# Optimization experiments

Measured on AMD Instinct MI355X. Metric: run time of the kernel, lower is better.

Reference implementation:

```python
import jax, jax.numpy as jnp
import numpy as np

N_R = 100_000   # real nodes
N_E = 1_200_000 # r2r edges
G = 4096        # graphs (= interaction nodes, one per graph)
H = 64          # hidden_dim
ND = 64         # node_dim
ED = 16         # edge_dim
L = 4           # conv_layers
TGT = 1         # target_dim
SLOPE = 0.1     # LeakyReLU negative slope used by ISATconv


def _seg_softmax(logits, seg, n):
    m = jax.ops.segment_max(logits, seg, num_segments=n)
    ex = jnp.exp(logits - m[seg])
    s = jax.ops.segment_sum(ex, seg, num_segments=n)
    return ex / s[seg]


def setup_inputs() -> dict:
    key = jax.random.key(0)
    ks = jax.random.split(key, 20)
    inp = {}
    inp['r_node'] = jax.random.normal(ks[0], (N_R, ND), jnp.float32)
    inp['i_node'] = jax.random.normal(ks[1], (G, 1), jnp.float32)
    inp['r_edge'] = jax.random.normal(ks[2], (N_E, ED), jnp.float32)
    inp['d_edge'] = jax.random.uniform(ks[3], (N_R, 1), jnp.float32)
    inp['r2r_src'] = jax.random.randint(ks[4], (N_E,), 0, N_R, jnp.int32)
    inp['r2r_dst'] = jax.random.randint(ks[5], (N_E,), 0, N_R, jnp.int32)
    inp['graph_id'] = jnp.sort(jax.random.randint(ks[6], (N_R,), 0, G, jnp.int32))
    sc = 1.0 / np.sqrt(H)
    inp['W_r'] = jax.random.normal(ks[7], (ND, H), jnp.float32) * (1.0 / np.sqrt(ND))
    inp['W_i'] = jax.random.normal(ks[8], (1, H), jnp.float32)
    inp['W_e'] = jax.random.normal(ks[9], (ED, H), jnp.float32) * (1.0 / np.sqrt(ED))
    inp['Wm'] = jax.random.normal(ks[10], (L, H, H), jnp.float32) * sc
    inp['a_s'] = jax.random.normal(ks[11], (L, H), jnp.float32) * sc
    inp['a_d'] = jax.random.normal(ks[12], (L, H), jnp.float32) * sc
    inp['a_e'] = jax.random.normal(ks[13], (L, H), jnp.float32) * sc
    inp['w_d'] = jax.random.normal(ks[14], (1,), jnp.float32)
    inp['b_d'] = jnp.zeros((1,), jnp.float32)
    inp['W_mlp'] = jax.random.normal(ks[15], (3, H, H), jnp.float32) * sc
    inp['b_mlp'] = jnp.zeros((3, H), jnp.float32)
    inp['W_out'] = jax.random.normal(ks[16], (H, TGT), jnp.float32) * sc
    inp['b_out'] = jnp.zeros((TGT,), jnp.float32)
    return inp


def reference(r_node, i_node, r_edge, d_edge, r2r_src, r2r_dst, graph_id,
              W_r, W_i, W_e, Wm, a_s, a_d, a_e, w_d, b_d,
              W_mlp, b_mlp, W_out, b_out):
    lrelu = lambda x: jax.nn.leaky_relu(x, SLOPE)
    n = r_node.shape[0]
    g = i_node.shape[0]
    # embeddings (bias-free linears)
    h = r_node @ W_r          # [N,H]
    hi = i_node @ W_i         # [G,H]
    e = r_edge @ W_e          # [E,H]
    score = None
    # ISAT attention conv layers (gather-compute-scatter), residual
    for l in range(L):
        logits = lrelu(h[r2r_src] @ a_s[l] + h[r2r_dst] @ a_d[l] + e @ a_e[l])  # [E]
        attn = _seg_softmax(logits, r2r_dst, n)
        msg = attn[:, None] * (h[r2r_src] + e)
        agg = jax.ops.segment_sum(msg, r2r_dst, num_segments=n) @ Wm[l]
        h = lrelu(h + agg)
        score = attn
    # interaction-node (d2d) mixing: gate by d_edge, gather to i-nodes, broadcast back
    gate = jax.nn.sigmoid(d_edge * w_d + b_d)                 # [N,1]
    hi = hi + jax.ops.segment_sum(gate * h, graph_id, num_segments=g)
    h = h + gate * hi[graph_id]
    # sum pooling over real-node subgraph per graph
    pooled = jax.ops.segment_sum(h, graph_id, num_segments=g)  # [G,H]
    # MLP readout: 3 hidden ReLU layers + linear output
    x = pooled
    for i in range(3):
        x = jax.nn.relu(x @ W_mlp[i] + b_mlp[i])
    return x @ W_out + b_out
```

## Files before the change

### kernel.cpp

```cpp
#include <hip/hip_runtime.h>
#include <math.h>

#define N_RN 100000
#define N_ED 1200000
#define N_G  4096
#define SCAN_CH 256
#define SCAN_NB ((N_RN + SCAN_CH - 1) / SCAN_CH)

__device__ __forceinline__ float lrelu(float x) { return x > 0.f ? x : 0.1f * x; }

__global__ void k_embed_h(const float* __restrict__ r_node,
                          const float* __restrict__ W_r,
                          const float* __restrict__ a_s0,
                          const float* __restrict__ a_d0,
                          float* __restrict__ h,
                          float* __restrict__ hs, float* __restrict__ hd) {
    __shared__ float Wl[64 * 64];
    __shared__ float arow[4][64];
    int tid = threadIdx.x;
    for (int i = tid; i < 4096; i += 256) Wl[i] = W_r[i];
    __syncthreads();
    int lane = tid & 63, w = tid >> 6;
    float asj = a_s0[lane], adj = a_d0[lane];
    int wid = blockIdx.x * 4 + w;
    int nw = gridDim.x * 4;
    for (int n = wid; n < N_RN; n += nw) {
        arow[w][lane] = r_node[(size_t)n * 64 + lane];
        float acc = 0.f;
#pragma unroll
        for (int d4 = 0; d4 < 16; ++d4) {
            float4 a = *(const float4*)&arow[w][d4 * 4];
            int d = d4 * 4;
            acc += a.x * Wl[(d + 0) * 64 + lane];
            acc += a.y * Wl[(d + 1) * 64 + lane];
            acc += a.z * Wl[(d + 2) * 64 + lane];
            acc += a.w * Wl[(d + 3) * 64 + lane];
        }
        h[(size_t)n * 64 + lane] = acc;
        float x = acc * asj, y = acc * adj;
#pragma unroll
        for (int off = 32; off; off >>= 1) {
            x += __shfl_xor(x, off, 64);
            y += __shfl_xor(y, off, 64);
        }
        if (lane == 0) { hs[n] = x; hd[n] = y; }
    }
}

__global__ void k_wewm(const float* __restrict__ W_e,
                       const float* __restrict__ Wm,
                       const float* __restrict__ a_e,
                       float* __restrict__ WeWm,
                       float* __restrict__ was_all) {
    int idx = blockIdx.x * blockDim.x + threadIdx.x;
    if (idx < 4096) {
        int l = idx >> 10, rem = idx & 1023;
        int t = rem >> 6, j = rem & 63;
        float acc = 0.f;
        for (int d = 0; d < 64; ++d)
            acc += W_e[t * 64 + d] * Wm[l * 4096 + d * 64 + j];
        WeWm[idx] = acc;
    } else {
        int r = idx - 4096;
        if (r < 64) {
            int l = r >> 4, t = r & 15;
            float acc = 0.f;
            for (int j = 0; j < 64; ++j)
                acc += W_e[t * 64 + j] * a_e[l * 64 + j];
            was_all[r] = acc;
        }
    }
}

__global__ void k_hist(const int* __restrict__ dst, int* __restrict__ deg) {
    int k = blockIdx.x * blockDim.x + threadIdx.x;
    if (k < N_ED) atomicAdd(deg + dst[k], 1);
}

__global__ void k_scan_a(const int* __restrict__ deg, int* __restrict__ bsum) {
    __shared__ int lds[SCAN_CH];
    int b = blockIdx.x, t = threadIdx.x;
    int i = b * SCAN_CH + t;
    int v = (i < N_RN) ? deg[i] : 0;
    lds[t] = v;
    __syncthreads();
    for (int d = 128; d; d >>= 1) {
        if (t < d) lds[t] += lds[t + d];
        __syncthreads();
    }
    if (t == 0) bsum[b] = lds[0];
}

__global__ void k_scan_b(int* __restrict__ bsum) {
    __shared__ int lds[512];
    int t = threadIdx.x;
    int v = (t < SCAN_NB) ? bsum[t] : 0;
    lds[t] = v;
    __syncthreads();
    for (int d = 1; d < 512; d <<= 1) {
        int u = (t >= d) ? lds[t - d] : 0;
        __syncthreads();
        lds[t] += u;
        __syncthreads();
    }
    if (t < SCAN_NB) bsum[t] = lds[t] - v;
}

__global__ void k_scan_c(const int* __restrict__ deg, const int* __restrict__ bsum,
                         int* __restrict__ off, int* __restrict__ cur) {
    __shared__ int lds[SCAN_CH];
    int b = blockIdx.x, t = threadIdx.x;
    int i = b * SCAN_CH + t;
    int v = (i < N_RN) ? deg[i] : 0;
    lds[t] = v;
    __syncthreads();
    for (int d = 1; d < SCAN_CH; d <<= 1) {
        int u = (t >= d) ? lds[t - d] : 0;
        __syncthreads();
        lds[t] += u;
        __syncthreads();
    }
    if (i < N_RN) {
        int incl = bsum[b] + lds[t];
        off[i + 1] = incl;
        cur[i] = incl - v;
        if (i == 0) off[0] = 0;
    }
}

__global__ void k_scatter(const float* __restrict__ r_edge,
                          const int* __restrict__ src, const int* __restrict__ dst,
                          int* __restrict__ cur,
                          int* __restrict__ src_perm,
                          float* __restrict__ r16_perm) {
    int k = blockIdx.x * blockDim.x + threadIdx.x;
    if (k >= N_ED) return;
    const float4* row = (const float4*)(r_edge + (size_t)k * 16);
    float4 r0 = row[0], r1 = row[1], r2 = row[2], r3 = row[3];
    int pos = atomicAdd(cur + dst[k], 1);
    src_perm[pos] = src[k];
    float4* o = (float4*)(r16_perm + (size_t)pos * 16);
    o[0] = r0; o[1] = r1; o[2] = r2; o[3] = r3;
}

__global__ void k_layer(const float* __restrict__ h_in,
                        const float* __restrict__ hs, const float* __restrict__ hd,
                        const int* __restrict__ off,
                        const int* __restrict__ src_perm,
                        const float* __restrict__ r16_perm,
                        const float* __restrict__ was_l,
                        const float* __restrict__ Wm_l,
                        const float* __restrict__ WeWm_l,
                        const float* __restrict__ a_s_n, const float* __restrict__ a_d_n,
                        float* __restrict__ h_out,
                        float* __restrict__ hs_out, float* __restrict__ hd_out) {
    __shared__ float Wl[64 * 64];
    __shared__ float Ww[16 * 64];
    __shared__ float arow[4][64];
    __shared__ float rrow[4][16];
    __shared__ float wbuf[4][64];
    __shared__ int   skbuf[4][64];
    int tid = threadIdx.x;
    for (int i = tid; i < 4096; i += 256) Wl[i] = Wm_l[i];
    for (int i = tid; i < 1024; i += 256) Ww[i] = WeWm_l[i];
    __syncthreads();
    int lane = tid & 63, w = tid >> 6;
    int g = lane >> 4, lg = lane & 15;
    float asj = a_s_n[lane], adj = a_d_n[lane];
    float wr[16];
#pragma unroll
    for (int t = 0; t < 16; ++t) wr[t] = was_l[t];
    int wid = blockIdx.x * 4 + w;
    int nw = gridDim.x * 4;
    for (int n = wid; n < N_RN; n += nw) {
        int base = off[n], end = off[n + 1];
        float hdn = hd[n];
        float m = -1e38f;
        float s = 0.f, racc = 0.f;
        float acc0 = 0.f, acc1 = 0.f, acc2 = 0.f, acc3 = 0.f;
        for (int cb = base; cb < end; cb += 64) {
            int cend = cb + 64 < end ? cb + 64 : end;
            int cnt = cend - cb;
            int pos = cb + lane;
            float lgt = -1e38f;
            int sk = 0;
            if (pos < cend) {
                sk = src_perm[pos];
                const float4* rp = (const float4*)(r16_perm + (size_t)pos * 16);
                float4 r0 = rp[0], r1 = rp[1], r2 = rp[2], r3 = rp[3];
                float ep = r0.x * wr[0] + r0.y * wr[1] + r0.z * wr[2] + r0.w * wr[3]
                         + r1.x * wr[4] + r1.y * wr[5] + r1.z * wr[6] + r1.w * wr[7]
                         + r2.x * wr[8] + r2.y * wr[9] + r2.z * wr[10] + r2.w * wr[11]
                         + r3.x * wr[12] + r3.y * wr[13] + r3.z * wr[14] + r3.w * wr[15];
                lgt = lrelu(hs[sk] + hdn + ep);
            }
            float cm = lgt;
#pragma unroll
            for (int o = 32; o; o >>= 1) cm = fmaxf(cm, __shfl_xor(cm, o, 64));
            float newm = fmaxf(m, cm);
            float scale = (m > -1e37f) ? __expf(m - newm) : 0.f;
            s *= scale; racc *= scale;
            acc0 *= scale; acc1 *= scale; acc2 *= scale; acc3 *= scale;
            m = newm;
            float wv = (pos < cend) ? __expf(lgt - m) : 0.f;
            s += wv;
            wbuf[w][lane] = wv;
            skbuf[w][lane] = sk;
            for (int c = 0; c < cnt; c += 4) {
                int e = c + g;
                if (e < cnt) {
                    float wgt = wbuf[w][e];
                    int sk2 = skbuf[w][e];
                    const float4 hv = *(const float4*)(h_in + (size_t)sk2 * 64 + (lg << 2));
                    acc0 += wgt * hv.x; acc1 += wgt * hv.y;
                    acc2 += wgt * hv.z; acc3 += wgt * hv.w;
                    racc += wgt * r16_perm[(size_t)(cb + e) * 16 + lg];
                }
            }
        }
        acc0 += __shfl_xor(acc0, 16, 64); acc0 += __shfl_xor(acc0, 32, 64);
        acc1 += __shfl_xor(acc1, 16, 64); acc1 += __shfl_xor(acc1, 32, 64);
        acc2 += __shfl_xor(acc2, 16, 64); acc2 += __shfl_xor(acc2, 32, 64);
        acc3 += __shfl_xor(acc3, 16, 64); acc3 += __shfl_xor(acc3, 32, 64);
        racc += __shfl_xor(racc, 16, 64); racc += __shfl_xor(racc, 32, 64);
#pragma unroll
        for (int o = 32; o; o >>= 1) s += __shfl_xor(s, o, 64);
        float inv = (end > base) ? 1.f / s : 0.f;
        if (g == 0) {
            float4 av = { acc0 * inv, acc1 * inv, acc2 * inv, acc3 * inv };
            *(float4*)&arow[w][lg << 2] = av;
            rrow[w][lg] = racc * inv;
        }
        float mm = 0.f;
#pragma unroll
        for (int d4 = 0; d4 < 16; ++d4) {
            float4 a = *(const float4*)&arow[w][d4 * 4];
            int d = d4 * 4;
            mm += a.x * Wl[(d + 0) * 64 + lane];
            mm += a.y * Wl[(d + 1) * 64 + lane];
            mm += a.z * Wl[(d + 2) * 64 + lane];
            mm += a.w * Wl[(d + 3) * 64 + lane];
        }
#pragma unroll
        for (int t = 0; t < 16; ++t) mm += rrow[w][t] * Ww[t * 64 + lane];
        size_t idx = (size_t)n * 64 + lane;
        float hv = lrelu(h_in[idx] + mm);
        h_out[idx] = hv;
        float x = hv * asj, y = hv * adj;
#pragma unroll
        for (int o = 32; o; o >>= 1) {
            x += __shfl_xor(x, o, 64);
            y += __shfl_xor(y, o, 64);
        }
        if (lane == 0) { hs_out[n] = x; hd_out[n] = y; }
    }
}

__global__ void k_readout(const float* __restrict__ h,
                          const float* __restrict__ d_edge,
                          const int* __restrict__ graph_id,
                          const float* __restrict__ i_node,
                          const float* __restrict__ W_i,
                          const float* __restrict__ w_d,
                          const float* __restrict__ b_d,
                          const float* __restrict__ W_mlp,
                          const float* __restrict__ b_mlp,
                          const float* __restrict__ W_out,
                          const float* __restrict__ b_out,
                          float* __restrict__ out) {
    int g = blockIdx.x, j = threadIdx.x;
    int lo = 0, hi = N_RN;
    while (lo < hi) { int mid = (lo + hi) >> 1; if (graph_id[mid] < g) lo = mid + 1; else hi = mid; }
    int start = lo;
    hi = N_RN;
    while (lo < hi) { int mid = (lo + hi) >> 1; if (graph_id[mid] < g + 1) lo = mid + 1; else hi = mid; }
    int end = lo;

    float wd = w_d[0], bd = b_d[0];
    float acc0 = 0.f, acc1 = 0.f, sg = 0.f;
    for (int n = start; n < end; ++n) {
        float hv = h[(size_t)n * 64 + j];
        float de = d_edge[n];
        float gate = 1.f / (1.f + __expf(-(de * wd + bd)));
        acc0 += hv;
        acc1 += gate * hv;
        sg += gate;
    }
    float hij = i_node[g] * W_i[j] + acc1;
    float pooled = acc0 + sg * hij;

    __shared__ float xa[64], xb[64];
    xa[j] = pooled;
    __syncthreads();
#pragma unroll
    for (int layer = 0; layer < 3; ++layer) {
        const float* W = W_mlp + layer * 4096;
        float* srcb = (layer & 1) ? xb : xa;
        float* dstb = (layer & 1) ? xa : xb;
        float acc = b_mlp[layer * 64 + j];
        for (int d = 0; d < 64; ++d) acc += srcb[d] * W[d * 64 + j];
        acc = fmaxf(acc, 0.f);
        __syncthreads();
        dstb[j] = acc;
        __syncthreads();
    }
    float v = xb[j] * W_out[j];
#pragma unroll
    for (int off = 32; off; off >>= 1) v += __shfl_xor(v, off, 64);
    if (j == 0) out[g] = v + b_out[0];
}

extern "C" void kernel_launch(void* const* d_in, const int* in_sizes, int n_in,
                              void* d_out, int out_size, void* d_ws, size_t ws_size,
                              hipStream_t stream) {
    const float* r_node  = (const float*)d_in[0];
    const float* i_node  = (const float*)d_in[1];
    const float* r_edge  = (const float*)d_in[2];
    const float* d_edge  = (const float*)d_in[3];
    const int*   r2r_src = (const int*)d_in[4];
    const int*   r2r_dst = (const int*)d_in[5];
    const int*   graph_id= (const int*)d_in[6];
    const float* W_r     = (const float*)d_in[7];
    const float* W_i     = (const float*)d_in[8];
    const float* W_e     = (const float*)d_in[9];
    const float* Wm      = (const float*)d_in[10];
    const float* a_s     = (const float*)d_in[11];
    const float* a_d     = (const float*)d_in[12];
    const float* a_e     = (const float*)d_in[13];
    const float* w_d     = (const float*)d_in[14];
    const float* b_d     = (const float*)d_in[15];
    const float* W_mlp   = (const float*)d_in[16];
    const float* b_mlp   = (const float*)d_in[17];
    const float* W_out   = (const float*)d_in[18];
    const float* b_out   = (const float*)d_in[19];
    float* out = (float*)d_out;

    float* ws = (float*)d_ws;
    float* h0   = ws;
    float* h1   = h0 + (size_t)N_RN * 64;
    float* hs0  = h1 + (size_t)N_RN * 64;
    float* hd0  = hs0 + N_RN;
    float* hs1  = hd0 + N_RN;
    float* hd1  = hs1 + N_RN;
    float* WeWm = hd1 + N_RN;
    float* wasb = WeWm + 4096;
    int*   deg  = (int*)(wasb + 64);
    int*   offs = deg + N_RN;
    int*   cur  = offs + N_RN + 1;
    int*   bsum = cur + N_RN;
    int*   src_perm = bsum + 512;
    float* r16_perm = (float*)(src_perm + N_ED);

    k_embed_h<<<2048, 256, 0, stream>>>(r_node, W_r, a_s, a_d, h0, hs0, hd0);
    k_wewm<<<17, 256, 0, stream>>>(W_e, Wm, a_e, WeWm, wasb);

    hipMemsetAsync(deg, 0, N_RN * sizeof(int), stream);
    k_hist<<<(N_ED + 255) / 256, 256, 0, stream>>>(r2r_dst, deg);
    k_scan_a<<<SCAN_NB, SCAN_CH, 0, stream>>>(deg, bsum);
    k_scan_b<<<1, 512, 0, stream>>>(bsum);
    k_scan_c<<<SCAN_NB, SCAN_CH, 0, stream>>>(deg, bsum, offs, cur);
    k_scatter<<<(N_ED + 255) / 256, 256, 0, stream>>>(r_edge, r2r_src, r2r_dst,
                                                      cur, src_perm, r16_perm);

    float* hin = h0;  float* hout = h1;
    float* hsi = hs0; float* hdi = hd0;
    float* hso = hs1; float* hdo = hd1;
    for (int l = 0; l < 4; ++l) {
        int ln = (l + 1) & 3;
        k_layer<<<2048, 256, 0, stream>>>(hin, hsi, hdi, offs, src_perm, r16_perm,
                                          wasb + l * 16, Wm + l * 4096, WeWm + l * 1024,
                                          a_s + ln * 64, a_d + ln * 64,
                                          hout, hso, hdo);
        float* t;
        t = hin; hin = hout; hout = t;
        t = hsi; hsi = hso; hso = t;
        t = hdi; hdi = hdo; hdo = t;
    }

    k_readout<<<N_G, 64, 0, stream>>>(hin, d_edge, graph_id, i_node, W_i, w_d, b_d,
                                      W_mlp, b_mlp, W_out, b_out, out);
}
```

Measured before the change: 874.4 us.

## Precompute h·Wm per node before aggregation instead of after

Uses linearity of the aggregation to transform node features by Wm once per node in a separate kernel, then gathers the pre-multiplied rows in the layer kernel. This removes the 16KB Wm shared-memory tile and the per-node 64x64 matvec from the layer kernel, which may raise occupancy. In exchange it adds an extra kernel launch per layer and an extra full read and write of the 100k×64 feature array. The arithmetic is the same up to floating-point reassociation.

```diff
diff --git a/kernel.cpp b/kernel.cpp
--- a/kernel.cpp
+++ b/kernel.cpp
@@ -44,6 +44,33 @@
             y += __shfl_xor(y, off, 64);
         }
         if (lane == 0) { hs[n] = x; hd[n] = y; }
+    }
+}
+
+__global__ void k_hwm(const float* __restrict__ h,
+                      const float* __restrict__ Wm_l,
+                      float* __restrict__ hWm) {
+    __shared__ float Wl[64 * 64];
+    __shared__ float arow[4][64];
+    int tid = threadIdx.x;
+    for (int i = tid; i < 4096; i += 256) Wl[i] = Wm_l[i];
+    __syncthreads();
+    int lane = tid & 63, w = tid >> 6;
+    int wid = blockIdx.x * 4 + w;
+    int nw = gridDim.x * 4;
+    for (int n = wid; n < N_RN; n += nw) {
+        arow[w][lane] = h[(size_t)n * 64 + lane];
+        float acc = 0.f;
+#pragma unroll
+        for (int d4 = 0; d4 < 16; ++d4) {
+            float4 a = *(const float4*)&arow[w][d4 * 4];
+            int d = d4 * 4;
+            acc += a.x * Wl[(d + 0) * 64 + lane];
+            acc += a.y * Wl[(d + 1) * 64 + lane];
+            acc += a.z * Wl[(d + 2) * 64 + lane];
+            acc += a.w * Wl[(d + 3) * 64 + lane];
+        }
+        hWm[(size_t)n * 64 + lane] = acc;
     }
 }
 
@@ -144,24 +171,22 @@
 }
 
 __global__ void k_layer(const float* __restrict__ h_in,
+                        const float* __restrict__ hWm,
                         const float* __restrict__ hs, const float* __restrict__ hd,
                         const int* __restrict__ off,
                         const int* __restrict__ src_perm,
                         const float* __restrict__ r16_perm,
                         const float* __restrict__ was_l,
-                        const float* __restrict__ Wm_l,
                         const float* __restrict__ WeWm_l,
                         const float* __restrict__ a_s_n, const float* __restrict__ a_d_n,
                         float* __restrict__ h_out,
                         float* __restrict__ hs_out, float* __restrict__ hd_out) {
-    __shared__ float Wl[64 * 64];
     __shared__ float Ww[16 * 64];
     __shared__ float arow[4][64];
     __shared__ float rrow[4][16];
     __shared__ float wbuf[4][64];
     __shared__ int   skbuf[4][64];
     int tid = threadIdx.x;
-    for (int i = tid; i < 4096; i += 256) Wl[i] = Wm_l[i];
     for (int i = tid; i < 1024; i += 256) Ww[i] = WeWm_l[i];
     __syncthreads();
     int lane = tid & 63, w = tid >> 6;
@@ -211,7 +236,7 @@
                 if (e < cnt) {
                     float wgt = wbuf[w][e];
                     int sk2 = skbuf[w][e];
-                    const float4 hv = *(const float4*)(h_in + (size_t)sk2 * 64 + (lg << 2));
+                    const float4 hv = *(const float4*)(hWm + (size_t)sk2 * 64 + (lg << 2));
                     acc0 += wgt * hv.x; acc1 += wgt * hv.y;
                     acc2 += wgt * hv.z; acc3 += wgt * hv.w;
                     racc += wgt * r16_perm[(size_t)(cb + e) * 16 + lg];
@@ -231,16 +256,7 @@
             *(float4*)&arow[w][lg << 2] = av;
             rrow[w][lg] = racc * inv;
         }
-        float mm = 0.f;
-#pragma unroll
-        for (int d4 = 0; d4 < 16; ++d4) {
-            float4 a = *(const float4*)&arow[w][d4 * 4];
-            int d = d4 * 4;
-            mm += a.x * Wl[(d + 0) * 64 + lane];
-            mm += a.y * Wl[(d + 1) * 64 + lane];
-            mm += a.z * Wl[(d + 2) * 64 + lane];
-            mm += a.w * Wl[(d + 3) * 64 + lane];
-        }
+        float mm = arow[w][lane];
 #pragma unroll
         for (int t = 0; t < 16; ++t) mm += rrow[w][t] * Ww[t * 64 + lane];
         size_t idx = (size_t)n * 64 + lane;
@@ -338,7 +354,8 @@
     float* ws = (float*)d_ws;
     float* h0   = ws;
     float* h1   = h0 + (size_t)N_RN * 64;
-    float* hs0  = h1 + (size_t)N_RN * 64;
+    float* hwm  = h1 + (size_t)N_RN * 64;
+    float* hs0  = hwm + (size_t)N_RN * 64;
     float* hd0  = hs0 + N_RN;
     float* hs1  = hd0 + N_RN;
     float* hd1  = hs1 + N_RN;
@@ -367,8 +384,9 @@
     float* hso = hs1; float* hdo = hd1;
     for (int l = 0; l < 4; ++l) {
         int ln = (l + 1) & 3;
-        k_layer<<<2048, 256, 0, stream>>>(hin, hsi, hdi, offs, src_perm, r16_perm,
-                                          wasb + l * 16, Wm + l * 4096, WeWm + l * 1024,
+        k_hwm<<<2048, 256, 0, stream>>>(hin, Wm + l * 4096, hwm);
+        k_layer<<<2048, 256, 0, stream>>>(hin, hwm, hsi, hdi, offs, src_perm, r16_perm,
+                                          wasb + l * 16, WeWm + l * 1024,
                                           a_s + ln * 64, a_d + ln * 64,
                                           hout, hso, hdo);
         float* t;
```

New measurement: 924.2 us. 1.06x slower.

## Process four destination nodes per wavefront with 16-lane subgroups in layer kernel

Applied to the files above, without the earlier changes.

The attention layer kernel now assigns four destination nodes to each 64-lane wavefront, one per 16-lane subgroup, in place of one node per wavefront. Edge chunks shrink to 16, and weights and source indices are broadcast with subgroup shuffles, which removes the LDS staging buffers. The dense 64x64 projection is computed with float4 outputs per lane. With an average of about 12 edges per node, the old layout left most of each 64-wide chunk idle, and this change targets that waste. The cost is divergence from the loop running to the maximum chunk count of the four nodes, plus different block sizing (1024x512).

```diff
diff --git a/kernel.cpp b/kernel.cpp
--- a/kernel.cpp
+++ b/kernel.cpp
@@ -154,37 +154,44 @@
                         const float* __restrict__ a_s_n, const float* __restrict__ a_d_n,
                         float* __restrict__ h_out,
                         float* __restrict__ hs_out, float* __restrict__ hd_out) {
-    __shared__ float Wl[64 * 64];
-    __shared__ float Ww[16 * 64];
-    __shared__ float arow[4][64];
-    __shared__ float rrow[4][16];
-    __shared__ float wbuf[4][64];
-    __shared__ int   skbuf[4][64];
+    __shared__ float Wl[4096];
+    __shared__ float Ww[1024];
+    __shared__ float arow[8][4 * 68 + 4];
     int tid = threadIdx.x;
-    for (int i = tid; i < 4096; i += 256) Wl[i] = Wm_l[i];
-    for (int i = tid; i < 1024; i += 256) Ww[i] = WeWm_l[i];
+    for (int i = tid; i < 4096; i += 512) Wl[i] = Wm_l[i];
+    for (int i = tid; i < 1024; i += 512) Ww[i] = WeWm_l[i];
     __syncthreads();
     int lane = tid & 63, w = tid >> 6;
     int g = lane >> 4, lg = lane & 15;
-    float asj = a_s_n[lane], adj = a_d_n[lane];
     float wr[16];
 #pragma unroll
     for (int t = 0; t < 16; ++t) wr[t] = was_l[t];
-    int wid = blockIdx.x * 4 + w;
-    int nw = gridDim.x * 4;
-    for (int n = wid; n < N_RN; n += nw) {
-        int base = off[n], end = off[n + 1];
-        float hdn = hd[n];
-        float m = -1e38f;
-        float s = 0.f, racc = 0.f;
-        float acc0 = 0.f, acc1 = 0.f, acc2 = 0.f, acc3 = 0.f;
-        for (int cb = base; cb < end; cb += 64) {
-            int cend = cb + 64 < end ? cb + 64 : end;
-            int cnt = cend - cb;
-            int pos = cb + lane;
+    float4 as4 = *(const float4*)&a_s_n[lg << 2];
+    float4 ad4 = *(const float4*)&a_d_n[lg << 2];
+    int Wv = blockIdx.x * 8 + w;
+    int NW = gridDim.x * 8;
+    for (int nb = Wv * 4; nb < N_RN; nb += NW * 4) {
+        int n = nb + g;
+        bool nact = n < N_RN;
+        int base = 0, end = 0;
+        if (nact) { base = off[n]; end = off[n + 1]; }
+        float hdn = nact ? hd[n] : 0.f;
+        float m = -1e38f, s = 0.f, racc = 0.f;
+        float ax = 0.f, ay = 0.f, az = 0.f, aw = 0.f;
+        int nch = (end - base + 15) >> 4;
+        int nmax = nch;
+        nmax = max(nmax, __shfl_xor(nmax, 16, 64));
+        nmax = max(nmax, __shfl_xor(nmax, 32, 64));
+        for (int c = 0; c < nmax; ++c) {
+            int cb = base + (c << 4);
+            int rem = end - cb;
+            int cnt = rem > 16 ? 16 : (rem > 0 ? rem : 0);
             float lgt = -1e38f;
+            float wvv = 0.f;
             int sk = 0;
-            if (pos < cend) {
+            bool act = lg < cnt;
+            if (act) {
+                int pos = cb + lg;
                 sk = src_perm[pos];
                 const float4* rp = (const float4*)(r16_perm + (size_t)pos * 16);
                 float4 r0 = rp[0], r1 = rp[1], r2 = rp[2], r3 = rp[3];
@@ -195,64 +202,85 @@
                 lgt = lrelu(hs[sk] + hdn + ep);
             }
             float cm = lgt;
-#pragma unroll
-            for (int o = 32; o; o >>= 1) cm = fmaxf(cm, __shfl_xor(cm, o, 64));
+            cm = fmaxf(cm, __shfl_xor(cm, 1, 16));
+            cm = fmaxf(cm, __shfl_xor(cm, 2, 16));
+            cm = fmaxf(cm, __shfl_xor(cm, 4, 16));
+            cm = fmaxf(cm, __shfl_xor(cm, 8, 16));
             float newm = fmaxf(m, cm);
             float scale = (m > -1e37f) ? __expf(m - newm) : 0.f;
             s *= scale; racc *= scale;
-            acc0 *= scale; acc1 *= scale; acc2 *= scale; acc3 *= scale;
+            ax *= scale; ay *= scale; az *= scale; aw *= scale;
             m = newm;
-            float wv = (pos < cend) ? __expf(lgt - m) : 0.f;
-            s += wv;
-            wbuf[w][lane] = wv;
-            skbuf[w][lane] = sk;
-            for (int c = 0; c < cnt; c += 4) {
-                int e = c + g;
-                if (e < cnt) {
-                    float wgt = wbuf[w][e];
-                    int sk2 = skbuf[w][e];
-                    const float4 hv = *(const float4*)(h_in + (size_t)sk2 * 64 + (lg << 2));
-                    acc0 += wgt * hv.x; acc1 += wgt * hv.y;
-                    acc2 += wgt * hv.z; acc3 += wgt * hv.w;
-                    racc += wgt * r16_perm[(size_t)(cb + e) * 16 + lg];
-                }
+            if (act) wvv = __expf(lgt - m);
+            s += wvv;
+            int e = 0;
+            for (; e + 1 < cnt; e += 2) {
+                float wgt0 = __shfl(wvv, e, 16);
+                int   sk0  = __shfl(sk, e, 16);
+                float wgt1 = __shfl(wvv, e + 1, 16);
+                int   sk1  = __shfl(sk, e + 1, 16);
+                const float4 h0v = *(const float4*)(h_in + (size_t)sk0 * 64 + (lg << 2));
+                const float4 h1v = *(const float4*)(h_in + (size_t)sk1 * 64 + (lg << 2));
+                float q0 = r16_perm[(size_t)(cb + e) * 16 + lg];
+                float q1 = r16_perm[(size_t)(cb + e + 1) * 16 + lg];
+                ax += wgt0 * h0v.x + wgt1 * h1v.x;
+                ay += wgt0 * h0v.y + wgt1 * h1v.y;
+                az += wgt0 * h0v.z + wgt1 * h1v.z;
+                aw += wgt0 * h0v.w + wgt1 * h1v.w;
+                racc += wgt0 * q0 + wgt1 * q1;
             }
-        }
-        acc0 += __shfl_xor(acc0, 16, 64); acc0 += __shfl_xor(acc0, 32, 64);
-        acc1 += __shfl_xor(acc1, 16, 64); acc1 += __shfl_xor(acc1, 32, 64);
-        acc2 += __shfl_xor(acc2, 16, 64); acc2 += __shfl_xor(acc2, 32, 64);
-        acc3 += __shfl_xor(acc3, 16, 64); acc3 += __shfl_xor(acc3, 32, 64);
-        racc += __shfl_xor(racc, 16, 64); racc += __shfl_xor(racc, 32, 64);
-#pragma unroll
-        for (int o = 32; o; o >>= 1) s += __shfl_xor(s, o, 64);
+            if (e < cnt) {
+                float wgt0 = __shfl(wvv, e, 16);
+                int   sk0  = __shfl(sk, e, 16);
+                const float4 h0v = *(const float4*)(h_in + (size_t)sk0 * 64 + (lg << 2));
+                float q0 = r16_perm[(size_t)(cb + e) * 16 + lg];
+                ax += wgt0 * h0v.x; ay += wgt0 * h0v.y;
+                az += wgt0 * h0v.z; aw += wgt0 * h0v.w;
+                racc += wgt0 * q0;
+            }
+        }
+        s += __shfl_xor(s, 1, 16);
+        s += __shfl_xor(s, 2, 16);
+        s += __shfl_xor(s, 4, 16);
+        s += __shfl_xor(s, 8, 16);
         float inv = (end > base) ? 1.f / s : 0.f;
-        if (g == 0) {
-            float4 av = { acc0 * inv, acc1 * inv, acc2 * inv, acc3 * inv };
-            *(float4*)&arow[w][lg << 2] = av;
-            rrow[w][lg] = racc * inv;
-        }
-        float mm = 0.f;
+        float* ar = &arow[w][g * 68];
+        *(float4*)&ar[lg << 2] = make_float4(ax * inv, ay * inv, az * inv, aw * inv);
+        float mx = 0.f, my = 0.f, mz = 0.f, mw = 0.f;
 #pragma unroll
         for (int d4 = 0; d4 < 16; ++d4) {
-            float4 a = *(const float4*)&arow[w][d4 * 4];
-            int d = d4 * 4;
-            mm += a.x * Wl[(d + 0) * 64 + lane];
-            mm += a.y * Wl[(d + 1) * 64 + lane];
-            mm += a.z * Wl[(d + 2) * 64 + lane];
-            mm += a.w * Wl[(d + 3) * 64 + lane];
-        }
-#pragma unroll
-        for (int t = 0; t < 16; ++t) mm += rrow[w][t] * Ww[t * 64 + lane];
-        size_t idx = (size_t)n * 64 + lane;
-        float hv = lrelu(h_in[idx] + mm);
-        h_out[idx] = hv;
-        float x = hv * asj, y = hv * adj;
-#pragma unroll
-        for (int o = 32; o; o >>= 1) {
-            x += __shfl_xor(x, o, 64);
-            y += __shfl_xor(y, o, 64);
-        }
-        if (lane == 0) { hs_out[n] = x; hd_out[n] = y; }
+            float4 a = *(const float4*)&ar[d4 << 2];
+            const float* wl = &Wl[(d4 << 2) * 64 + (lg << 2)];
+            float4 w0 = *(const float4*)&wl[0];
+            float4 w1 = *(const float4*)&wl[64];
+            float4 w2 = *(const float4*)&wl[128];
+            float4 w3 = *(const float4*)&wl[192];
+            mx += a.x * w0.x + a.y * w1.x + a.z * w2.x + a.w * w3.x;
+            my += a.x * w0.y + a.y * w1.y + a.z * w2.y + a.w * w3.y;
+            mz += a.x * w0.z + a.y * w1.z + a.z * w2.z + a.w * w3.z;
+            mw += a.x * w0.w + a.y * w1.w + a.z * w2.w + a.w * w3.w;
+        }
+        float rs = racc * inv;
+#pragma unroll
+        for (int t = 0; t < 16; ++t) {
+            float rt = __shfl(rs, t, 16);
+            const float4 wt = *(const float4*)&Ww[t * 64 + (lg << 2)];
+            mx += rt * wt.x; my += rt * wt.y; mz += rt * wt.z; mw += rt * wt.w;
+        }
+        if (nact) {
+            const float4 hi4 = *(const float4*)(h_in + (size_t)n * 64 + (lg << 2));
+            float4 hv;
+            hv.x = lrelu(hi4.x + mx); hv.y = lrelu(hi4.y + my);
+            hv.z = lrelu(hi4.z + mz); hv.w = lrelu(hi4.w + mw);
+            *(float4*)(h_out + (size_t)n * 64 + (lg << 2)) = hv;
+            float x = hv.x * as4.x + hv.y * as4.y + hv.z * as4.z + hv.w * as4.w;
+            float y = hv.x * ad4.x + hv.y * ad4.y + hv.z * ad4.z + hv.w * ad4.w;
+            x += __shfl_xor(x, 1, 16); x += __shfl_xor(x, 2, 16);
+            x += __shfl_xor(x, 4, 16); x += __shfl_xor(x, 8, 16);
+            y += __shfl_xor(y, 1, 16); y += __shfl_xor(y, 2, 16);
+            y += __shfl_xor(y, 4, 16); y += __shfl_xor(y, 8, 16);
+            if (lg == 0) { hs_out[n] = x; hd_out[n] = y; }
+        }
     }
 }
 
@@ -367,7 +395,7 @@
     float* hso = hs1; float* hdo = hd1;
     for (int l = 0; l < 4; ++l) {
         int ln = (l + 1) & 3;
-        k_layer<<<2048, 256, 0, stream>>>(hin, hsi, hdi, offs, src_perm, r16_perm,
+        k_layer<<<1024, 512, 0, stream>>>(hin, hsi, hdi, offs, src_perm, r16_perm,
                                           wasb + l * 16, Wm + l * 4096, WeWm + l * 1024,
                                           a_s + ln * 64, a_d + ln * 64,
                                           hout, hso, hdo);
```

Result: faster. 729.6 us (-16.6%).
